# Optimization experiments

Measured on AMD Instinct MI355X. Metric: run time of the kernel, lower is better.

The kernel has to match this reference:

```python
import jax, jax.numpy as jnp
import numpy as np

VOCAB = 50257
INPUT_DIM = 1024
CUTOFF_ENDS = [0, 10000, 30000, VOCAB]
PROJ_DIMS = [1024, 512, 256]  # input_dim // factor**i, factor=2.0
N_TOKENS = 8192


def setup_inputs() -> dict:
    key = jax.random.key(0)
    ks = jax.random.split(key, 16)
    inp = {
        "x": jax.random.normal(ks[0], (N_TOKENS, INPUT_DIM), dtype=jnp.float32),
        "target": jax.random.randint(ks[1], (N_TOKENS,), 0, VOCAB, dtype=jnp.int64),
    }
    # Per-cluster projection weights (nn.Linear(input_dim, proj_dim, bias=False) -> [proj_dim, input_dim])
    # and output layers (nn.Linear(proj_dim, cluster_size) -> weight [cluster, proj_dim], bias [cluster]).
    for i in range(3):
        cluster = CUTOFF_ENDS[i + 1] - CUTOFF_ENDS[i]
        pd = PROJ_DIMS[i]
        inp[f"p{i}"] = jax.random.normal(ks[2 + 3 * i], (pd, INPUT_DIM), dtype=jnp.float32) * 0.02
        inp[f"w{i}"] = jax.random.normal(ks[3 + 3 * i], (cluster, pd), dtype=jnp.float32) * 0.02
        inp[f"b{i}"] = jnp.zeros((cluster,), dtype=jnp.float32)
    return inp


def reference(x, target, p0, w0, b0, p1, w1, b1, p2, w2, b2):
    # Faithful to torch AdaptiveSoftmax.forward(input, target):
    # per-cluster: gather tokens whose target falls in [l, r), project, classify,
    # cross-entropy. Clusters partition [0, vocab), so every token hits exactly
    # one cluster; we compute each cluster's pipeline densely over all tokens
    # (jit-friendly, no data-dependent shapes) and select per-token via the mask.
    projs, ws, bs = [p0, p1, p2], [w0, w1, w2], [b0, b1, b2]
    target = target.astype(jnp.int32)
    nll = jnp.zeros((x.shape[0],), dtype=x.dtype)
    for i in range(3):
        l, r = CUTOFF_ENDS[i], CUTOFF_ENDS[i + 1]
        mask = (target >= l) & (target < r)
        hidden = jnp.einsum('nd,pd->np', x, projs[i])          # [N, proj_dim]
        logits = jnp.einsum('np,cp->nc', hidden, ws[i]) + bs[i]  # [N, cluster]
        logp = jax.nn.log_softmax(logits, axis=-1)
        t_i = jnp.clip(target - l, 0, r - l - 1)
        nll_i = -jnp.take_along_axis(logp, t_i[:, None], axis=1)[:, 0]
        nll = jnp.where(mask, nll_i, nll)
    loss = nll.sum()  # == sum of per-cluster reduction='sum' cross-entropies
    return loss, nll
```

## Files before the change

### kernel.cpp

```cpp
#include <hip/hip_runtime.h>
#include <cmath>

#define N_TOK 8192
#define DIM 1024

using bf16x8 = __attribute__((ext_vector_type(8))) short;
using f32x4  = __attribute__((ext_vector_type(4))) float;

__device__ __forceinline__ unsigned f2bf(float f) {
  unsigned u = __float_as_uint(f);
  return (u + 0x7fffu + ((u >> 16) & 1u)) >> 16;
}

__device__ __forceinline__ void gll16(const void* g, void* l) {
  __builtin_amdgcn_global_load_lds(
      (const __attribute__((address_space(1))) void*)g,
      (__attribute__((address_space(3))) void*)l, 16, 0, 0);
}

__global__ __launch_bounds__(1024) void k_setup(const int* __restrict__ tgt,
                                                int* __restrict__ cnt,
                                                int* __restrict__ hoff,
                                                int* __restrict__ perm,
                                                float* __restrict__ psum) {
  __shared__ int base[3];
  int t = threadIdx.x;
  if (t < 3) base[t] = 0;
  __syncthreads();
  for (int i = t; i < N_TOK; i += 1024) {
    int tg = tgt[i];
    int cid = (tg < 10000) ? 0 : (tg < 30000 ? 1 : 2);
    int slot = atomicAdd(&base[cid], 1);
    perm[cid * N_TOK + slot] = i;
  }
  for (int i = t; i < N_TOK; i += 1024) psum[i] = 0.f;
  __syncthreads();
  if (t < 3) cnt[t] = base[t];
  if (t == 0) {
    hoff[0] = 0;
    hoff[1] = base[0] * 1024;
    hoff[2] = base[0] * 1024 + base[1] * 512;
  }
}

__global__ __launch_bounds__(256) void k_hc(
    const float* __restrict__ x,
    const float* __restrict__ p0, const float* __restrict__ p1, const float* __restrict__ p2,
    const float* __restrict__ w0, const float* __restrict__ w1, const float* __restrict__ w2,
    const int* __restrict__ perm, const int* __restrict__ cnt, const int* __restrict__ hoffs,
    unsigned short* __restrict__ wb, unsigned short* __restrict__ hb) {
  if (blockIdx.z == 0) {
    const int nw0 = 10240000, nw1 = 10240000, nw2 = 5185792;
    const int total4 = (nw0 + nw1 + nw2) >> 2;
    for (int i = blockIdx.x * 256 + threadIdx.x; i < total4; i += 512 * 256) {
      int e = i << 2;
      const float* src;
      if (e < nw0) src = w0 + e;
      else if (e < nw0 + nw1) src = w1 + (e - nw0);
      else src = w2 + (e - nw0 - nw1);
      float4 v = *(const float4*)src;
      uint2 o;
      o.x = f2bf(v.x) | (f2bf(v.y) << 16);
      o.y = f2bf(v.z) | (f2bf(v.w) << 16);
      *(uint2*)(wb + e) = o;
    }
    return;
  }
  const int cid = blockIdx.z - 1;
  const int pd = (cid == 0) ? 1024 : (cid == 1) ? 512 : 256;
  const int count = cnt[cid];
  if (count == 0) return;
  const int nchd = pd >> 7;
  const int chunk = blockIdx.x % nchd;
  const int tile = blockIdx.x / nchd;
  if (tile * 128 >= count) return;
  const int dim0 = chunk * 128, row0 = tile * 128;
  const float* P = (cid == 0) ? p0 : (cid == 1) ? p1 : p2;
  const size_t hoff = (size_t)hoffs[cid];

  __shared__ char pool[34816];
  __shared__ int ptoks[128];
  short* stg = (short*)pool;
  short* Os = (short*)pool;

  const int t = threadIdx.x, wv = t >> 6, lane = t & 63, m = lane & 15, q = lane >> 4;
  const int wr = wv >> 1, wc = wv & 1;

  if (t < 128) {
    int idx = row0 + t;
    ptoks[t] = perm[cid * N_TOK + min(idx, count - 1)];
  }
  __syncthreads();

  const int s0 = t, s1 = t + 256;
  const int r0 = s0 >> 2, g0 = (s0 & 3) ^ ((r0 >> 1) & 3);
  const int r1 = s1 >> 2, g1 = (s1 & 3) ^ ((r1 >> 1) & 3);
  const uint4* srcA0 = (const uint4*)(x + (size_t)ptoks[r0] * DIM) + g0 * 2;
  const uint4* srcA1 = (const uint4*)(x + (size_t)ptoks[r1] * DIM) + g1 * 2;
  const uint4* srcB0 = (const uint4*)(P + (size_t)(dim0 + r0) * DIM) + g0 * 2;
  const uint4* srcB1 = (const uint4*)(P + (size_t)(dim0 + r1) * DIM) + g1 * 2;

  f32x4 acc[4][4];
  #pragma unroll
  for (int rt = 0; rt < 4; ++rt)
    #pragma unroll
    for (int ct = 0; ct < 4; ++ct) acc[rt][ct] = (f32x4){0.f, 0.f, 0.f, 0.f};

  const int sR = (q ^ ((m >> 1) & 3)) * 8;

  {
    uint4 a0 = srcA0[0], a1 = srcA0[1], a2 = srcA1[0], a3 = srcA1[1];
    uint4 b0 = srcB0[0], b1 = srcB0[1], b2 = srcB1[0], b3 = srcB1[1];
    uint4 o;
    o.x = (a0.x >> 16) | (a0.y & 0xFFFF0000u); o.y = (a0.z >> 16) | (a0.w & 0xFFFF0000u);
    o.z = (a1.x >> 16) | (a1.y & 0xFFFF0000u); o.w = (a1.z >> 16) | (a1.w & 0xFFFF0000u);
    *(uint4*)&stg[s0 * 8] = o;
    o.x = (a2.x >> 16) | (a2.y & 0xFFFF0000u); o.y = (a2.z >> 16) | (a2.w & 0xFFFF0000u);
    o.z = (a3.x >> 16) | (a3.y & 0xFFFF0000u); o.w = (a3.z >> 16) | (a3.w & 0xFFFF0000u);
    *(uint4*)&stg[s1 * 8] = o;
    o.x = (b0.x >> 16) | (b0.y & 0xFFFF0000u); o.y = (b0.z >> 16) | (b0.w & 0xFFFF0000u);
    o.z = (b1.x >> 16) | (b1.y & 0xFFFF0000u); o.w = (b1.z >> 16) | (b1.w & 0xFFFF0000u);
    *(uint4*)&stg[4096 + s0 * 8] = o;
    o.x = (b2.x >> 16) | (b2.y & 0xFFFF0000u); o.y = (b2.z >> 16) | (b2.w & 0xFFFF0000u);
    o.z = (b3.x >> 16) | (b3.y & 0xFFFF0000u); o.w = (b3.z >> 16) | (b3.w & 0xFFFF0000u);
    *(uint4*)&stg[4096 + s1 * 8] = o;
  }

  int p = 0;
  for (int ks = 0; ks < 32; ++ks) {
    __syncthreads();
    const bool nxt = (ks + 1) < 32;
    uint4 a0, a1, a2, a3, b0, b1, b2, b3;
    if (nxt) {
      int ko = (ks + 1) * 8;
      a0 = srcA0[ko]; a1 = srcA0[ko + 1]; a2 = srcA1[ko]; a3 = srcA1[ko + 1];
      b0 = srcB0[ko]; b1 = srcB0[ko + 1]; b2 = srcB1[ko]; b3 = srcB1[ko + 1];
    }
    short* SAp = stg + p * 8192;
    short* SBp = SAp + 4096;
    bf16x8 af[4];
    #pragma unroll
    for (int rt = 0; rt < 4; ++rt)
      af[rt] = *(bf16x8*)&SAp[(wr * 64 + rt * 16 + m) * 32 + sR];
    #pragma unroll
    for (int ct = 0; ct < 4; ++ct) {
      bf16x8 bb = *(bf16x8*)&SBp[(wc * 64 + ct * 16 + m) * 32 + sR];
      #pragma unroll
      for (int rt = 0; rt < 4; ++rt)
        acc[rt][ct] = __builtin_amdgcn_mfma_f32_16x16x32_bf16(af[rt], bb, acc[rt][ct], 0, 0, 0);
    }
    if (nxt) {
      short* DA = stg + (p ^ 1) * 8192;
      short* DB = DA + 4096;
      uint4 o;
      o.x = (a0.x >> 16) | (a0.y & 0xFFFF0000u); o.y = (a0.z >> 16) | (a0.w & 0xFFFF0000u);
      o.z = (a1.x >> 16) | (a1.y & 0xFFFF0000u); o.w = (a1.z >> 16) | (a1.w & 0xFFFF0000u);
      *(uint4*)&DA[s0 * 8] = o;
      o.x = (a2.x >> 16) | (a2.y & 0xFFFF0000u); o.y = (a2.z >> 16) | (a2.w & 0xFFFF0000u);
      o.z = (a3.x >> 16) | (a3.y & 0xFFFF0000u); o.w = (a3.z >> 16) | (a3.w & 0xFFFF0000u);
      *(uint4*)&DA[s1 * 8] = o;
      o.x = (b0.x >> 16) | (b0.y & 0xFFFF0000u); o.y = (b0.z >> 16) | (b0.w & 0xFFFF0000u);
      o.z = (b1.x >> 16) | (b1.y & 0xFFFF0000u); o.w = (b1.z >> 16) | (b1.w & 0xFFFF0000u);
      *(uint4*)&DB[s0 * 8] = o;
      o.x = (b2.x >> 16) | (b2.y & 0xFFFF0000u); o.y = (b2.z >> 16) | (b2.w & 0xFFFF0000u);
      o.z = (b3.x >> 16) | (b3.y & 0xFFFF0000u); o.w = (b3.z >> 16) | (b3.w & 0xFFFF0000u);
      *(uint4*)&DB[s1 * 8] = o;
    }
    p ^= 1;
  }

  __syncthreads();
  #pragma unroll
  for (int rt = 0; rt < 4; ++rt)
    #pragma unroll
    for (int ct = 0; ct < 4; ++ct)
      #pragma unroll
      for (int rr = 0; rr < 4; ++rr)
        Os[(wr * 64 + rt * 16 + q * 4 + rr) * 136 + wc * 64 + ct * 16 + m] =
            (short)f2bf(acc[rt][ct][rr]);
  __syncthreads();
  {
    int orow = t >> 1, oh = t & 1;
    int slot = row0 + orow;
    if (slot < count) {
      unsigned short* dst = hb + hoff + (size_t)slot * pd + dim0 + oh * 64;
      const short* src = &Os[orow * 136 + oh * 64];
      #pragma unroll
      for (int i = 0; i < 8; ++i)
        *(uint4*)(dst + i * 8) = *(const uint4*)(src + i * 8);
    }
  }
}

__global__ __launch_bounds__(256, 2) void k_lse(
    const unsigned short* __restrict__ hb, const unsigned short* __restrict__ wb,
    const float* __restrict__ b0_, const float* __restrict__ b1_, const float* __restrict__ b2_,
    const int* __restrict__ tgt, const int* __restrict__ perm,
    const int* __restrict__ cnt, const int* __restrict__ hoffs,
    float* __restrict__ psum, float* __restrict__ tlog) {
  const int cid = blockIdx.z;
  const int pd     = (cid == 0) ? 1024  : (cid == 1) ? 512   : 256;
  const int cstart = (cid == 0) ? 0     : (cid == 1) ? 10000 : 30000;
  const int csize  = (cid == 0) ? 10000 : (cid == 1) ? 20000 : 20257;
  const size_t woff = (cid == 0) ? 0 : (cid == 1) ? (size_t)10240000 : (size_t)20480000;
  const float* bias = (cid == 0) ? b0_ : (cid == 1) ? b1_ : b2_;
  const int count = cnt[cid];
  if (count == 0) return;
  const unsigned ntile = (unsigned)(count + 127) >> 7;
  const int nchunk = (csize + 255) >> 8;
  const int cpx = (nchunk + 7) >> 3;

  const unsigned d = blockIdx.x;
  const int x8 = d & 7;
  const unsigned g = d >> 3;
  const unsigned ci = g / ntile;
  if (ci >= (unsigned)cpx) return;
  const int chunk = x8 * cpx + (int)ci;
  if (chunk >= nchunk) return;
  const int tile = (int)(g - ci * ntile);
  const int col0 = chunk * 256, row0 = tile * 128;
  const size_t hoff = (size_t)hoffs[cid];

  __shared__ char pool[73728];
  short* SAs = (short*)pool;
  short* SBs = (short*)(pool + 24576);

  const int t = threadIdx.x, wv = t >> 6, lane = t & 63, m = lane & 15, q = lane >> 4;
  const int wr = wv >> 1, wc = wv & 1;

  const int sub = lane >> 2;
  const int gsw = (lane & 3) ^ ((sub >> 1) & 3);
  const unsigned short *pA[2], *pB[4];
  int aOff[2], bOff[4];
  #pragma unroll
  for (int i = 0; i < 2; ++i) {
    int ia = wv * 2 + i;
    int ra = ia * 16 + sub;
    aOff[i] = ia * 512;
    pA[i] = hb + hoff + (size_t)min(row0 + ra, count - 1) * pd + gsw * 8;
  }
  #pragma unroll
  for (int j = 0; j < 4; ++j) {
    int ib = wv * 4 + j;
    int rb = ib * 16 + sub;
    bOff[j] = ib * 512;
    pB[j] = wb + woff + (size_t)min(col0 + rb, csize - 1) * pd + gsw * 8;
  }

  f32x4 acc[4][8];
  #pragma unroll
  for (int rt = 0; rt < 4; ++rt)
    #pragma unroll
    for (int ct = 0; ct < 8; ++ct) acc[rt][ct] = (f32x4){0.f, 0.f, 0.f, 0.f};

  const int sR = (q ^ ((m >> 1) & 3)) * 8;
  const int nk = pd >> 5;

  #pragma unroll
  for (int i = 0; i < 2; ++i) gll16(pA[i], SAs + aOff[i]);
  #pragma unroll
  for (int j = 0; j < 4; ++j) gll16(pB[j], SBs + bOff[j]);
  #pragma unroll
  for (int i = 0; i < 2; ++i) gll16(pA[i] + 32, SAs + 4096 + aOff[i]);
  #pragma unroll
  for (int j = 0; j < 4; ++j) gll16(pB[j] + 32, SBs + 8192 + bOff[j]);

  int p = 0;
  for (int ks = 0; ks < nk; ++ks) {
    if (ks + 1 < nk) asm volatile("s_waitcnt vmcnt(6)" ::: "memory");
    else             asm volatile("s_waitcnt vmcnt(0)" ::: "memory");
    __builtin_amdgcn_s_barrier();
    asm volatile("" ::: "memory");
    if (ks + 2 < nk) {
      const int ko = (ks + 2) * 32;
      const int pn = (p == 0) ? 2 : p - 1;
      #pragma unroll
      for (int i = 0; i < 2; ++i) gll16(pA[i] + ko, SAs + pn * 4096 + aOff[i]);
      #pragma unroll
      for (int j = 0; j < 4; ++j) gll16(pB[j] + ko, SBs + pn * 8192 + bOff[j]);
    }
    const int pbA = p * 4096, pbB = p * 8192;
    bf16x8 af[4];
    #pragma unroll
    for (int rt = 0; rt < 4; ++rt)
      af[rt] = *(bf16x8*)&SAs[pbA + (wr * 64 + rt * 16 + m) * 32 + sR];
    #pragma unroll
    for (int ct = 0; ct < 8; ++ct) {
      bf16x8 bb = *(bf16x8*)&SBs[pbB + (wc * 128 + ct * 16 + m) * 32 + sR];
      #pragma unroll
      for (int rt = 0; rt < 4; ++rt)
        acc[rt][ct] = __builtin_amdgcn_mfma_f32_16x16x32_bf16(af[rt], bb, acc[rt][ct], 0, 0, 0);
    }
    p = (p == 2) ? 0 : p + 1;
  }
  asm volatile("" ::: "memory");

  __syncthreads();
  int* ptoks = (int*)pool;
  int* tlocs = (int*)(pool + 1024);
  if (t < 128) {
    int idx = row0 + t;
    int tok = perm[cid * N_TOK + min(idx, count - 1)];
    ptoks[t] = tok;
    tlocs[t] = tgt[tok] - cstart;
  }
  __syncthreads();

  float bc[8];
  #pragma unroll
  for (int ct = 0; ct < 8; ++ct)
    bc[ct] = bias[min(col0 + wc * 128 + ct * 16 + m, csize - 1)];

  int tl[4][4];
  #pragma unroll
  for (int rt = 0; rt < 4; ++rt)
    #pragma unroll
    for (int rr = 0; rr < 4; ++rr)
      tl[rt][rr] = tlocs[wr * 64 + rt * 16 + q * 4 + rr];

  float run[4][4] = {{0.f}}, tcap[4][4] = {{0.f}};
  int tfnd[4][4] = {{0}};

  #pragma unroll
  for (int ct = 0; ct < 8; ++ct) {
    int colg = col0 + wc * 128 + ct * 16 + m;
    bool cok = colg < csize;
    #pragma unroll
    for (int rt = 0; rt < 4; ++rt)
      #pragma unroll
      for (int rr = 0; rr < 4; ++rr) {
        float val = acc[rt][ct][rr] + bc[ct];
        if (cok) {
          run[rt][rr] += __expf(val);
          if (tl[rt][rr] == colg) { tcap[rt][rr] = val; tfnd[rt][rr] = 1; }
        }
      }
  }

  #pragma unroll
  for (int rt = 0; rt < 4; ++rt)
    #pragma unroll
    for (int rr = 0; rr < 4; ++rr) {
      float v = run[rt][rr];
      v += __shfl_xor(v, 1, 64);
      v += __shfl_xor(v, 2, 64);
      v += __shfl_xor(v, 4, 64);
      v += __shfl_xor(v, 8, 64);
      int rowl = wr * 64 + rt * 16 + q * 4 + rr;
      if (row0 + rowl < count) {
        int tok = ptoks[rowl];
        if (m == 0) atomicAdd(&psum[tok], v);
        if (tfnd[rt][rr]) tlog[tok] = tcap[rt][rr];
      }
    }
}

__global__ __launch_bounds__(1024) void k_final(const float* __restrict__ psum,
                                                const float* __restrict__ tlog,
                                                float* __restrict__ out) {
  __shared__ float part[16];
  int t = threadIdx.x;
  float s = 0.f;
  for (int n = t; n < N_TOK; n += 1024) {
    float v = __logf(psum[n]) - tlog[n];
    out[1 + n] = v;
    s += v;
  }
  #pragma unroll
  for (int off = 32; off > 0; off >>= 1) s += __shfl_down(s, off, 64);
  if ((t & 63) == 0) part[t >> 6] = s;
  __syncthreads();
  if (t < 64) {
    float v = (t < 16) ? part[t] : 0.f;
    #pragma unroll
    for (int off = 8; off > 0; off >>= 1) v += __shfl_down(v, off, 64);
    if (t == 0) out[0] = v;
  }
}

extern "C" void kernel_launch(void* const* d_in, const int* in_sizes, int n_in,
                              void* d_out, int out_size, void* d_ws, size_t ws_size,
                              hipStream_t stream) {
  const float* x  = (const float*)d_in[0];
  const int* tgt  = (const int*)d_in[1];
  const float* p0 = (const float*)d_in[2];
  const float* w0 = (const float*)d_in[3];
  const float* b0 = (const float*)d_in[4];
  const float* p1 = (const float*)d_in[5];
  const float* w1 = (const float*)d_in[6];
  const float* b1 = (const float*)d_in[7];
  const float* p2 = (const float*)d_in[8];
  const float* w2 = (const float*)d_in[9];
  const float* b2 = (const float*)d_in[10];
  float* out = (float*)d_out;

  char* ws = (char*)d_ws;
  int* cnt            = (int*)(ws + 0);
  int* hoff           = (int*)(ws + 64);
  int* perm           = (int*)(ws + 256);
  unsigned short* wb  = (unsigned short*)(ws + 131072);
  unsigned short* hb  = (unsigned short*)(ws + 51462656);
  float* psum         = (float*)(ws + 68239872);
  float* tlog         = (float*)(ws + 68272640);

  k_setup<<<dim3(1), dim3(1024), 0, stream>>>(tgt, cnt, hoff, perm, psum);
  k_hc<<<dim3(512, 1, 4), dim3(256), 0, stream>>>(x, p0, p1, p2, w0, w1, w2,
                                                  perm, cnt, hoff, wb, hb);
  k_lse<<<dim3(5120, 1, 3), dim3(256), 0, stream>>>(hb, wb, b0, b1, b2, tgt, perm, cnt, hoff,
                                                    psum, tlog);
  k_final<<<dim3(1), dim3(1024), 0, stream>>>(psum, tlog, out);
}
```

Baseline: 422.0 us.

## Pre-convert x and projections to bf16, stage projection GEMM via global_load_lds

After: 419.1 us. Within noise of the previous version (-0.7%).

```diff
diff --git a/kernel.cpp b/kernel.cpp
--- a/kernel.cpp
+++ b/kernel.cpp
@@ -18,34 +18,62 @@
       (__attribute__((address_space(3))) void*)l, 16, 0, 0);
 }
 
-__global__ __launch_bounds__(1024) void k_setup(const int* __restrict__ tgt,
-                                                int* __restrict__ cnt,
-                                                int* __restrict__ hoff,
-                                                int* __restrict__ perm,
-                                                float* __restrict__ psum) {
-  __shared__ int base[3];
-  int t = threadIdx.x;
-  if (t < 3) base[t] = 0;
-  __syncthreads();
-  for (int i = t; i < N_TOK; i += 1024) {
-    int tg = tgt[i];
-    int cid = (tg < 10000) ? 0 : (tg < 30000 ? 1 : 2);
-    int slot = atomicAdd(&base[cid], 1);
-    perm[cid * N_TOK + slot] = i;
-  }
-  for (int i = t; i < N_TOK; i += 1024) psum[i] = 0.f;
-  __syncthreads();
-  if (t < 3) cnt[t] = base[t];
-  if (t == 0) {
-    hoff[0] = 0;
-    hoff[1] = base[0] * 1024;
-    hoff[2] = base[0] * 1024 + base[1] * 512;
-  }
-}
-
-__global__ __launch_bounds__(256) void k_hc(
+__global__ __launch_bounds__(256) void k_pre(
+    const int* __restrict__ tgt,
     const float* __restrict__ x,
     const float* __restrict__ p0, const float* __restrict__ p1, const float* __restrict__ p2,
+    int* __restrict__ cnt, int* __restrict__ hoff, int* __restrict__ perm,
+    unsigned short* __restrict__ xb, unsigned short* __restrict__ pb,
+    float* __restrict__ psum) {
+  const int t = threadIdx.x;
+  if (blockIdx.x == 0) {
+    __shared__ int base[3];
+    if (t < 3) base[t] = 0;
+    __syncthreads();
+    for (int i = t; i < N_TOK; i += 256) {
+      int tg = tgt[i];
+      int cid = (tg < 10000) ? 0 : (tg < 30000 ? 1 : 2);
+      int slot = atomicAdd(&base[cid], 1);
+      perm[cid * N_TOK + slot] = i;
+    }
+    for (int i = t; i < N_TOK; i += 256) psum[i] = 0.f;
+    __syncthreads();
+    if (t < 3) cnt[t] = base[t];
+    if (t == 0) {
+      hoff[0] = 0;
+      hoff[1] = base[0] * 1024;
+      hoff[2] = base[0] * 1024 + base[1] * 512;
+    }
+    return;
+  }
+  const int nx4 = (N_TOK * DIM) >> 2;
+  const int np4 = ((1024 + 512 + 256) * DIM) >> 2;
+  const int n0 = 1024 * DIM, n1 = 512 * DIM;
+  for (int i = (blockIdx.x - 1) * 256 + t; i < nx4 + np4; i += 255 * 256) {
+    const float* src;
+    unsigned short* dst;
+    if (i < nx4) {
+      int e = i << 2;
+      src = x + e;
+      dst = xb + e;
+    } else {
+      int e = (i - nx4) << 2;
+      if (e < n0) src = p0 + e;
+      else if (e < n0 + n1) src = p1 + (e - n0);
+      else src = p2 + (e - n0 - n1);
+      dst = pb + e;
+    }
+    float4 v = *(const float4*)src;
+    uint2 o;
+    o.x = f2bf(v.x) | (f2bf(v.y) << 16);
+    o.y = f2bf(v.z) | (f2bf(v.w) << 16);
+    *(uint2*)dst = o;
+  }
+}
+
+__global__ __launch_bounds__(256) void k_hc(
+    const unsigned short* __restrict__ xb,
+    const unsigned short* __restrict__ pb,
     const float* __restrict__ w0, const float* __restrict__ w1, const float* __restrict__ w2,
     const int* __restrict__ perm, const int* __restrict__ cnt, const int* __restrict__ hoffs,
     unsigned short* __restrict__ wb, unsigned short* __restrict__ hb) {
@@ -75,12 +103,14 @@
   const int tile = blockIdx.x / nchd;
   if (tile * 128 >= count) return;
   const int dim0 = chunk * 128, row0 = tile * 128;
-  const float* P = (cid == 0) ? p0 : (cid == 1) ? p1 : p2;
+  const unsigned short* Pb =
+      pb + ((cid == 0) ? (size_t)0 : (cid == 1) ? (size_t)1048576 : (size_t)1572864);
   const size_t hoff = (size_t)hoffs[cid];
 
   __shared__ char pool[34816];
   __shared__ int ptoks[128];
-  short* stg = (short*)pool;
+  short* SA = (short*)pool;
+  short* SB = (short*)(pool + 16384);
   short* Os = (short*)pool;
 
   const int t = threadIdx.x, wv = t >> 6, lane = t & 63, m = lane & 15, q = lane >> 4;
@@ -92,13 +122,17 @@
   }
   __syncthreads();
 
-  const int s0 = t, s1 = t + 256;
-  const int r0 = s0 >> 2, g0 = (s0 & 3) ^ ((r0 >> 1) & 3);
-  const int r1 = s1 >> 2, g1 = (s1 & 3) ^ ((r1 >> 1) & 3);
-  const uint4* srcA0 = (const uint4*)(x + (size_t)ptoks[r0] * DIM) + g0 * 2;
-  const uint4* srcA1 = (const uint4*)(x + (size_t)ptoks[r1] * DIM) + g1 * 2;
-  const uint4* srcB0 = (const uint4*)(P + (size_t)(dim0 + r0) * DIM) + g0 * 2;
-  const uint4* srcB1 = (const uint4*)(P + (size_t)(dim0 + r1) * DIM) + g1 * 2;
+  const int sub = lane >> 2;
+  const int gsw = (lane & 3) ^ ((sub >> 1) & 3);
+  const unsigned short *pA[2], *pB[2];
+  int iaL[2];
+  #pragma unroll
+  for (int i = 0; i < 2; ++i) {
+    int ia = wv * 2 + i;
+    iaL[i] = ia * 512;
+    pA[i] = xb + (size_t)ptoks[ia * 16 + sub] * DIM + gsw * 8;
+    pB[i] = Pb + (size_t)(dim0 + ia * 16 + sub) * DIM + gsw * 8;
+  }
 
   f32x4 acc[4][4];
   #pragma unroll
@@ -108,63 +142,35 @@
 
   const int sR = (q ^ ((m >> 1) & 3)) * 8;
 
-  {
-    uint4 a0 = srcA0[0], a1 = srcA0[1], a2 = srcA1[0], a3 = srcA1[1];
-    uint4 b0 = srcB0[0], b1 = srcB0[1], b2 = srcB1[0], b3 = srcB1[1];
-    uint4 o;
-    o.x = (a0.x >> 16) | (a0.y & 0xFFFF0000u); o.y = (a0.z >> 16) | (a0.w & 0xFFFF0000u);
-    o.z = (a1.x >> 16) | (a1.y & 0xFFFF0000u); o.w = (a1.z >> 16) | (a1.w & 0xFFFF0000u);
-    *(uint4*)&stg[s0 * 8] = o;
-    o.x = (a2.x >> 16) | (a2.y & 0xFFFF0000u); o.y = (a2.z >> 16) | (a2.w & 0xFFFF0000u);
-    o.z = (a3.x >> 16) | (a3.y & 0xFFFF0000u); o.w = (a3.z >> 16) | (a3.w & 0xFFFF0000u);
-    *(uint4*)&stg[s1 * 8] = o;
-    o.x = (b0.x >> 16) | (b0.y & 0xFFFF0000u); o.y = (b0.z >> 16) | (b0.w & 0xFFFF0000u);
-    o.z = (b1.x >> 16) | (b1.y & 0xFFFF0000u); o.w = (b1.z >> 16) | (b1.w & 0xFFFF0000u);
-    *(uint4*)&stg[4096 + s0 * 8] = o;
-    o.x = (b2.x >> 16) | (b2.y & 0xFFFF0000u); o.y = (b2.z >> 16) | (b2.w & 0xFFFF0000u);
-    o.z = (b3.x >> 16) | (b3.y & 0xFFFF0000u); o.w = (b3.z >> 16) | (b3.w & 0xFFFF0000u);
-    *(uint4*)&stg[4096 + s1 * 8] = o;
+  #pragma unroll
+  for (int i = 0; i < 2; ++i) {
+    gll16(pA[i], SA + iaL[i]);
+    gll16(pB[i], SB + iaL[i]);
   }
 
   int p = 0;
   for (int ks = 0; ks < 32; ++ks) {
     __syncthreads();
-    const bool nxt = (ks + 1) < 32;
-    uint4 a0, a1, a2, a3, b0, b1, b2, b3;
-    if (nxt) {
-      int ko = (ks + 1) * 8;
-      a0 = srcA0[ko]; a1 = srcA0[ko + 1]; a2 = srcA1[ko]; a3 = srcA1[ko + 1];
-      b0 = srcB0[ko]; b1 = srcB0[ko + 1]; b2 = srcB1[ko]; b3 = srcB1[ko + 1];
-    }
-    short* SAp = stg + p * 8192;
-    short* SBp = SAp + 4096;
+    if (ks + 1 < 32) {
+      const int ko = (ks + 1) * 32;
+      const int bo = (p ^ 1) * 4096;
+      #pragma unroll
+      for (int i = 0; i < 2; ++i) {
+        gll16(pA[i] + ko, SA + bo + iaL[i]);
+        gll16(pB[i] + ko, SB + bo + iaL[i]);
+      }
+    }
+    const int pb_ = p * 4096;
     bf16x8 af[4];
     #pragma unroll
     for (int rt = 0; rt < 4; ++rt)
-      af[rt] = *(bf16x8*)&SAp[(wr * 64 + rt * 16 + m) * 32 + sR];
+      af[rt] = *(bf16x8*)&SA[pb_ + (wr * 64 + rt * 16 + m) * 32 + sR];
     #pragma unroll
     for (int ct = 0; ct < 4; ++ct) {
-      bf16x8 bb = *(bf16x8*)&SBp[(wc * 64 + ct * 16 + m) * 32 + sR];
+      bf16x8 bb = *(bf16x8*)&SB[pb_ + (wc * 64 + ct * 16 + m) * 32 + sR];
       #pragma unroll
       for (int rt = 0; rt < 4; ++rt)
         acc[rt][ct] = __builtin_amdgcn_mfma_f32_16x16x32_bf16(af[rt], bb, acc[rt][ct], 0, 0, 0);
-    }
-    if (nxt) {
-      short* DA = stg + (p ^ 1) * 8192;
-      short* DB = DA + 4096;
-      uint4 o;
-      o.x = (a0.x >> 16) | (a0.y & 0xFFFF0000u); o.y = (a0.z >> 16) | (a0.w & 0xFFFF0000u);
-      o.z = (a1.x >> 16) | (a1.y & 0xFFFF0000u); o.w = (a1.z >> 16) | (a1.w & 0xFFFF0000u);
-      *(uint4*)&DA[s0 * 8] = o;
-      o.x = (a2.x >> 16) | (a2.y & 0xFFFF0000u); o.y = (a2.z >> 16) | (a2.w & 0xFFFF0000u);
-      o.z = (a3.x >> 16) | (a3.y & 0xFFFF0000u); o.w = (a3.z >> 16) | (a3.w & 0xFFFF0000u);
-      *(uint4*)&DA[s1 * 8] = o;
-      o.x = (b0.x >> 16) | (b0.y & 0xFFFF0000u); o.y = (b0.z >> 16) | (b0.w & 0xFFFF0000u);
-      o.z = (b1.x >> 16) | (b1.y & 0xFFFF0000u); o.w = (b1.z >> 16) | (b1.w & 0xFFFF0000u);
-      *(uint4*)&DB[s0 * 8] = o;
-      o.x = (b2.x >> 16) | (b2.y & 0xFFFF0000u); o.y = (b2.z >> 16) | (b2.w & 0xFFFF0000u);
-      o.z = (b3.x >> 16) | (b3.y & 0xFFFF0000u); o.w = (b3.z >> 16) | (b3.w & 0xFFFF0000u);
-      *(uint4*)&DB[s1 * 8] = o;
     }
     p ^= 1;
   }
@@ -402,9 +408,12 @@
   unsigned short* hb  = (unsigned short*)(ws + 51462656);
   float* psum         = (float*)(ws + 68239872);
   float* tlog         = (float*)(ws + 68272640);
-
-  k_setup<<<dim3(1), dim3(1024), 0, stream>>>(tgt, cnt, hoff, perm, psum);
-  k_hc<<<dim3(512, 1, 4), dim3(256), 0, stream>>>(x, p0, p1, p2, w0, w1, w2,
+  unsigned short* xb  = (unsigned short*)(ws + 68305408);
+  unsigned short* pb  = (unsigned short*)(ws + 85082624);
+
+  k_pre<<<dim3(256), dim3(256), 0, stream>>>(tgt, x, p0, p1, p2,
+                                             cnt, hoff, perm, xb, pb, psum);
+  k_hc<<<dim3(512, 1, 4), dim3(256), 0, stream>>>(xb, pb, w0, w1, w2,
                                                   perm, cnt, hoff, wb, hb);
   k_lse<<<dim3(5120, 1, 3), dim3(256), 0, stream>>>(hb, wb, b0, b1, b2, tgt, perm, cnt, hoff,
                                                     psum, tlog);
```
